# Kernel optimization log

Measured on AMD Instinct MI355X. Metric: run time of the kernel, lower is better.

Reference implementation:

```python
import jax, jax.numpy as jnp
import numpy as np

S = 2048
HIDDEN = 4096
NH, NKV, HD = 32, 8, 128
QPK = NH // NKV  # 4
BLOCK, LOCAL, VERT = 64, 16, 8
ROPE_BASE = 1.0e6
SCALE = 1.0 / HD  # mup scaling: head_dim / mup_attn_multiplier(=1.0)


def setup_inputs() -> dict:
    key = jax.random.key(0)
    ks = jax.random.split(key, 5)
    qkv_out = NKV * (QPK + 2) * HD  # 6144, head-major layout
    return {
        "positions": jnp.arange(S, dtype=jnp.int32),
        "hidden_states": jax.random.normal(ks[0], (S, HIDDEN), jnp.float32),
        "w_qkv": jax.random.normal(ks[1], (qkv_out, HIDDEN), jnp.float32) * 0.02,
        "b_qkv": jax.random.normal(ks[2], (qkv_out,), jnp.float32) * 0.02,
        "w_dense": jax.random.normal(ks[3], (HIDDEN, HIDDEN), jnp.float32) * 0.02,
        "b_dense": jax.random.normal(ks[4], (HIDDEN,), jnp.float32) * 0.02,
    }


def _rope(x, cos, sin):
    # NeoX-style (non-interleaved) rotary over full head_dim.
    # x: [S, n_heads, HD]; cos/sin: [S, HD//2]
    d2 = x.shape[-1] // 2
    x1, x2 = x[..., :d2], x[..., d2:]
    c, s = cos[:, None, :], sin[:, None, :]
    return jnp.concatenate([x1 * c - x2 * s, x2 * c + x1 * s], axis=-1)


def _blocksparse_mask(positions):
    # vllm phi3small pattern: block (qb,kb) active iff causal AND
    # (qb-kb < local_blocks OR (kb + head + 1) % vert_stride == 0), hetero heads.
    qb = positions // BLOCK                       # [S]
    heads = jnp.arange(NH, dtype=positions.dtype)
    diff = qb[:, None] - qb[None, :]              # [S,S]
    local = diff < LOCAL                          # [S,S]
    vert = ((qb[None, None, :] + heads[:, None, None] + 1) % VERT) == 0  # [NH,1,S]
    causal = positions[:, None] >= positions[None, :]                     # [S,S]
    return (local[None] | vert) & causal[None]    # [NH,S,S]


def reference(positions, hidden_states, w_qkv, b_qkv, w_dense, b_dense):
    seq = hidden_states.shape[0]
    qkv = hidden_states @ w_qkv.T + b_qkv                   # [S, 6144]
    qkv = qkv.reshape(seq, NKV, QPK + 2, HD)                # head-major split
    q = qkv[:, :, :QPK].reshape(seq, NH, HD)
    k = qkv[:, :, QPK]                                      # [S, NKV, HD]
    v = qkv[:, :, QPK + 1]

    pos = positions.astype(jnp.float32)  # rope_position_scale = 1.0
    inv_freq = 1.0 / (ROPE_BASE ** (jnp.arange(0, HD, 2, dtype=jnp.float32) / HD))
    freqs = pos[:, None] * inv_freq                          # [S, HD/2]
    cos, sin = jnp.cos(freqs), jnp.sin(freqs)
    q = _rope(q, cos, sin)
    k = _rope(k, cos, sin)

    # GQA: each kv head serves QPK query heads
    kx = jnp.repeat(k, QPK, axis=1)                          # [S, NH, HD]
    vx = jnp.repeat(v, QPK, axis=1)

    scores = jnp.einsum('qhd,khd->hqk', q, kx) * SCALE       # [NH,S,S]
    mask = _blocksparse_mask(positions)
    scores = jnp.where(mask, scores, -jnp.inf)  # diag always in local block -> no empty rows
    p = jax.nn.softmax(scores, axis=-1)
    out = jnp.einsum('hqk,khd->qhd', p, vx).reshape(seq, NH * HD)
    return out @ w_dense.T + b_dense
```

## Files before the change

### kernel.cpp

```cpp
#include <hip/hip_runtime.h>

#define S_LEN   2048
#define HID     4096
#define NHEADS  32
#define NKVH    8
#define HDIM    128
#define NQKV    6144
#define ATT_SCALE (1.0f/128.0f)

typedef unsigned short u16;
typedef __attribute__((ext_vector_type(8))) __bf16 bf16x8;
typedef __attribute__((ext_vector_type(4))) float  f32x4;

__device__ __forceinline__ u16 f2bf(float f) {
    union { float f; unsigned u; } x; x.f = f;
    unsigned u = x.u;
    u += 0x7fffu + ((u >> 16) & 1u);
    return (u16)(u >> 16);
}
__device__ __forceinline__ float bf2f(u16 v) {
    union { unsigned u; float f; } x; x.u = ((unsigned)v) << 16; return x.f;
}

__global__ __launch_bounds__(256) void cvt_bf16_kernel(const float* __restrict__ in,
                                                       u16* __restrict__ out, int n4) {
    int stride = gridDim.x * blockDim.x;
    for (int i = blockIdx.x * blockDim.x + threadIdx.x; i < n4; i += stride) {
        float4 v = *(const float4*)(in + (size_t)i * 4);
        ushort4 o = make_ushort4(f2bf(v.x), f2bf(v.y), f2bf(v.z), f2bf(v.w));
        *(ushort4*)(out + (size_t)i * 4) = o;
    }
}

#define GFENCE() asm volatile("" ::: "memory")
#define GSBAR()  do { GFENCE(); __builtin_amdgcn_s_barrier(); GFENCE(); } while (0)

template <int BN_, int NB_, bool OUT_BF16>
__global__ __launch_bounds__(512, 2) void gemm_fc_kernel(
    const u16* __restrict__ A,
    const u16* __restrict__ B,
    const float* __restrict__ bias,
    void* __restrict__ Cout,
    int M, int N, int K)
{
    constexpr int LB = BN_ / 128;
    constexpr int VM = 2 + LB;
    __shared__ u16 lds[16384 + 2 * BN_ * 64];

    const int tid  = threadIdx.x;
    const int wid  = tid >> 6;
    const int lane = tid & 63;
    const int ln   = lane & 15;
    const int quad = lane >> 4;
    const int wr   = wid >> 2;
    const int wc   = wid & 3;
    const int tileM = blockIdx.y * 128;
    const int tileN = blockIdx.x * BN_;

    f32x4 acc[2][NB_][4];
    #pragma unroll
    for (int b = 0; b < 2; b++)
        #pragma unroll
        for (int n = 0; n < NB_; n++)
            #pragma unroll
            for (int m = 0; m < 4; m++) {
                f32x4 z = {0.f, 0.f, 0.f, 0.f};
                acc[b][n][m] = z;
            }

    const int srho = lane >> 3;
    const int scol = (((lane & 7) ^ srho) << 3);

    auto gload = [&](const u16* src, u16* dst) {
        __builtin_amdgcn_global_load_lds(
            (const __attribute__((address_space(1))) void*)src,
            (__attribute__((address_space(3))) void*)dst, 16, 0, 0);
    };
    auto stage_A = [&](int kk, int bb) {
        const int base = bb * 8192;
        #pragma unroll
        for (int s = 0; s < 2; s++) {
            const int rho0 = s * 64 + wid * 8;
            const int rho  = rho0 + srho;
            const u16* src = A + (size_t)(tileM + rho) * K + (size_t)kk * 64 + scol;
            gload(src, &lds[base + rho0 * 64]);
        }
    };
    auto stage_Bh = [&](int h, int kk, int bb) {
        const int base = 16384 + bb * (BN_ * 64) + h * ((BN_ / 2) * 64);
        #pragma unroll
        for (int s = 0; s < LB; s++) {
            const int rho0 = s * 64 + wid * 8;
            const int rho  = rho0 + srho;
            const u16* src = B + (size_t)(tileN + h * (BN_ / 2) + rho) * K
                               + (size_t)kk * 64 + scol;
            gload(src, &lds[base + rho0 * 64]);
        }
    };

#define WAIT_VM()                                                                   \
    do {                                                                            \
        if constexpr (VM == 5) asm volatile("s_waitcnt vmcnt(5)" ::: "memory");     \
        else                   asm volatile("s_waitcnt vmcnt(4)" ::: "memory");     \
    } while (0)

#define READ_A()                                                                    \
    do {                                                                            \
        _Pragma("unroll")                                                           \
        for (int m = 0; m < 4; m++) {                                               \
            const int ra = wr * 64 + m * 16 + ln;                                   \
            const int ab = buf * 8192 + ra * 64;                                    \
            const int rx = ra & 7;                                                  \
            af[m][0] = *(const bf16x8*)(&lds[ab + ((quad ^ rx) << 3)]);             \
            af[m][1] = *(const bf16x8*)(&lds[ab + (((4 + quad) ^ rx) << 3)]);       \
        }                                                                           \
    } while (0)

#define MFMA_B(b_)                                                                  \
    do {                                                                            \
        __builtin_amdgcn_s_setprio(1);                                              \
        _Pragma("unroll")                                                           \
        for (int n = 0; n < NB_; n++) {                                             \
            const int rb = (b_) * (BN_ / 2) + wc * (NB_ * 16) + n * 16 + ln;        \
            const int bb = 16384 + buf * (BN_ * 64) + rb * 64;                      \
            const int rx = rb & 7;                                                  \
            bf16x8 b0 = *(const bf16x8*)(&lds[bb + ((quad ^ rx) << 3)]);            \
            bf16x8 b1 = *(const bf16x8*)(&lds[bb + (((4 + quad) ^ rx) << 3)]);      \
            _Pragma("unroll")                                                       \
            for (int m = 0; m < 4; m++) {                                           \
                acc[b_][n][m] = __builtin_amdgcn_mfma_f32_16x16x32_bf16(            \
                    af[m][0], b0, acc[b_][n][m], 0, 0, 0);                          \
                acc[b_][n][m] = __builtin_amdgcn_mfma_f32_16x16x32_bf16(            \
                    af[m][1], b1, acc[b_][n][m], 0, 0, 0);                          \
            }                                                                       \
        }                                                                           \
        __builtin_amdgcn_s_setprio(0);                                              \
    } while (0)

    const int nIter = K / 64;

    stage_A(0, 0); stage_Bh(0, 0, 0); stage_Bh(1, 0, 0);

    bf16x8 af[4][2];

    for (int t = 0; t < nIter; t++) {
        const int buf = t & 1;
        const int bn  = buf ^ 1;
        const int kn  = (t + 1 == nIter) ? 0 : t + 1;

        stage_A(kn, bn);
        WAIT_VM();
        GSBAR();
        READ_A();
        MFMA_B(0);

        stage_Bh(0, kn, bn);
        WAIT_VM();
        GSBAR();
        MFMA_B(1);
        stage_Bh(1, kn, bn);

        asm volatile("s_waitcnt lgkmcnt(0)" ::: "memory");
        GSBAR();
    }

    asm volatile("s_waitcnt vmcnt(0)" ::: "memory");

#undef WAIT_VM
#undef READ_A
#undef MFMA_B

    #pragma unroll
    for (int b = 0; b < 2; b++)
        #pragma unroll
        for (int n = 0; n < NB_; n++) {
            const int col = tileN + b * (BN_ / 2) + wc * (NB_ * 16) + n * 16 + ln;
            const float bv = bias[col];
            #pragma unroll
            for (int m = 0; m < 4; m++) {
                #pragma unroll
                for (int r = 0; r < 4; r++) {
                    const int row = tileM + wr * 64 + m * 16 + quad * 4 + r;
                    float v = acc[b][n][m][r] + bv;
                    if (OUT_BF16)
                        ((u16*)Cout)[(size_t)row * N + col] = f2bf(v);
                    else
                        ((float*)Cout)[(size_t)row * N + col] = v;
                }
            }
        }
}

__global__ __launch_bounds__(128) void rope_split_kernel(
    const u16* __restrict__ qkv, const int* __restrict__ positions,
    u16* __restrict__ qb_o, u16* __restrict__ kb_o)
{
    const int d   = threadIdx.x;
    const int pos = blockIdx.x;
    const int hy  = blockIdx.y;
    const float p = (float)positions[pos];

    const u16* src;
    u16* dst;
    if (hy < NHEADS) {
        int kv = hy >> 2, qi = hy & 3;
        src = qkv + (size_t)pos * NQKV + (kv * 6 + qi) * HDIM;
        dst = qb_o + ((size_t)hy * S_LEN + pos) * HDIM;
    } else {
        int kv = hy - NHEADS;
        src = qkv + (size_t)pos * NQKV + (kv * 6 + 4) * HDIM;
        dst = kb_o + ((size_t)kv * S_LEN + pos) * HDIM;
    }
    int d2 = d & 63;
    float inv = expf(-(float)d2 * (13.815510557964274f / 64.0f));
    float fr = p * inv;
    float s, c;
    sincosf(fr, &s, &c);
    float x1 = bf2f(src[d2]);
    float x2 = bf2f(src[d2 + 64]);
    float o = (d < 64) ? (x1 * c - x2 * s) : (x2 * c + x1 * s);
    dst[d] = f2bf(o);
}

__global__ __launch_bounds__(256) void vtrans_kernel(
    const u16* __restrict__ qkv,
    u16* __restrict__ VT)
{
    __shared__ u16 T[64][HDIM + 8];
    const int s0 = blockIdx.x * 64;
    const int kv = blockIdx.y;
    const int tid = threadIdx.x;
    #pragma unroll
    for (int p = 0; p < 4; p++) {
        int pos = p * 16 + (tid >> 4);
        int d   = (tid & 15) * 8;
        *(uint4*)&T[pos][d] =
            *(const uint4*)(qkv + (size_t)(s0 + pos) * NQKV + (kv * 6 + 5) * HDIM + d);
    }
    __syncthreads();
    #pragma unroll
    for (int p = 0; p < 4; p++) {
        int d  = p * 32 + (tid >> 3);
        int sc = (tid & 7) * 8;
        u16 tmp[8];
        #pragma unroll
        for (int j = 0; j < 8; j++) tmp[j] = T[sc + j][d];
        *(uint4*)(VT + ((size_t)kv * HDIM + d) * S_LEN + s0 + sc) = *(uint4*)tmp;
    }
}

__global__ __launch_bounds__(512, 4) void attn_bs_kernel(
    const u16* __restrict__ Q,
    const u16* __restrict__ K,
    const u16* __restrict__ V,
    u16* __restrict__ O)
{
    __shared__ u16 Ks[64 * 128];
    __shared__ u16 Vt[128 * 64];
    __shared__ u16 Ps[8][16 * 64];

    const int blk = (int)gridDim.x - 1 - (int)blockIdx.x;
    const int h   = blockIdx.y;
    const int kv  = h >> 2;
    const int tid  = threadIdx.x;
    const int w    = tid >> 6;
    const int lane = tid & 63;
    const int ln   = lane & 15;
    const int quad = lane >> 4;
    const int qbw  = 2 * blk + (w >> 2);
    const int rb16 = (w & 3) * 16;

    bf16x8 aq[4];
    {
        const u16* Qg = Q + ((size_t)h * S_LEN + qbw * 64 + rb16 + ln) * HDIM + quad * 8;
        #pragma unroll
        for (int ks = 0; ks < 4; ks++)
            aq[ks] = *(const bf16x8*)(Qg + ks * 32);
    }

    f32x4 oacc[8];
    #pragma unroll
    for (int n = 0; n < 8; n++) { f32x4 z = {0.f,0.f,0.f,0.f}; oacc[n] = z; }
    float mrow[4] = {-1e30f, -1e30f, -1e30f, -1e30f};
    float lrow[4] = {0.f, 0.f, 0.f, 0.f};

    const int kbMax = 2 * blk + 1;
    for (int kb = 0; kb <= kbMax; kb++) {
        const bool vert = (((kb + h + 1) & 7) == 0);
        const bool selu = ((kbMax - kb) < 17) || vert;
        if (!selu) continue;

        __syncthreads();

        const u16* Kg  = K + ((size_t)kv * S_LEN + kb * 64) * HDIM;
        const u16* VTg = V + (size_t)kv * HDIM * S_LEN + kb * 64;

        #pragma unroll
        for (int p = 0; p < 2; p++) {
            int r0  = w * 8 + p * 4;
            int row = r0 + (lane >> 4);
            const u16* src = Kg + (size_t)row * HDIM + (((lane & 15) ^ (row & 7)) << 3);
            __builtin_amdgcn_global_load_lds(
                (const __attribute__((address_space(1))) void*)src,
                (__attribute__((address_space(3))) void*)&Ks[r0 * 128], 16, 0, 0);
        }
        #pragma unroll
        for (int p = 0; p < 2; p++) {
            int r0  = w * 16 + p * 8;
            int row = r0 + (lane >> 3);
            int c   = (lane & 7) ^ (row & 7);
            const u16* src = VTg + (size_t)row * S_LEN + c * 8;
            __builtin_amdgcn_global_load_lds(
                (const __attribute__((address_space(1))) void*)src,
                (__attribute__((address_space(3))) void*)&Vt[r0 * 64], 16, 0, 0);
        }
        __syncthreads();

        const bool mine = (kb <= qbw) && (((qbw - kb) < 16) || vert);
        if (mine) {
            f32x4 sacc[4];
            #pragma unroll
            for (int jj = 0; jj < 4; jj++) { f32x4 z = {0.f,0.f,0.f,0.f}; sacc[jj] = z; }
            __builtin_amdgcn_s_setprio(1);
            #pragma unroll
            for (int ks = 0; ks < 4; ks++) {
                #pragma unroll
                for (int jj = 0; jj < 4; jj++) {
                    bf16x8 bk = *(const bf16x8*)(
                        &Ks[(jj * 16 + ln) * 128 + (((ks * 4 + quad) ^ (ln & 7)) << 3)]);
                    sacc[jj] = __builtin_amdgcn_mfma_f32_16x16x32_bf16(aq[ks], bk, sacc[jj], 0, 0, 0);
                }
            }
            __builtin_amdgcn_s_setprio(0);

            const bool diag = (kb == qbw);
            float pv[4][4], mxr[4];
            bool grow = false;
            #pragma unroll
            for (int r = 0; r < 4; r++) {
                const int qrow = rb16 + quad * 4 + r;
                float mx = -1e30f;
                #pragma unroll
                for (int jj = 0; jj < 4; jj++) {
                    float s = sacc[jj][r] * ATT_SCALE;
                    if (diag && (jj * 16 + ln) > qrow) s = -1e30f;
                    pv[r][jj] = s;
                    mx = fmaxf(mx, s);
                }
                #pragma unroll
                for (int off = 1; off < 16; off <<= 1)
                    mx = fmaxf(mx, __shfl_xor(mx, off, 64));
                mxr[r] = mx;
                grow |= (mx > mrow[r] + 8.0f);
            }
            if (__any(grow)) {
                #pragma unroll
                for (int r = 0; r < 4; r++) {
                    float mnew  = fmaxf(mrow[r], mxr[r]);
                    float alpha = __expf(mrow[r] - mnew);
                    lrow[r] *= alpha;
                    mrow[r]  = mnew;
                    #pragma unroll
                    for (int n = 0; n < 8; n++) oacc[n][r] *= alpha;
                }
            }
            #pragma unroll
            for (int r = 0; r < 4; r++) {
                float sum = 0.f;
                #pragma unroll
                for (int jj = 0; jj < 4; jj++) {
                    float pe = __expf(pv[r][jj] - mrow[r]);
                    pv[r][jj] = pe;
                    sum += pe;
                }
                #pragma unroll
                for (int off = 1; off < 16; off <<= 1)
                    sum += __shfl_xor(sum, off, 64);
                lrow[r] += sum;
                const int prow = quad * 4 + r;
                #pragma unroll
                for (int jj = 0; jj < 4; jj++)
                    Ps[w][prow * 64 + (((jj * 2 + (ln >> 3)) ^ (prow & 7)) << 3) + (ln & 7)]
                        = f2bf(pv[r][jj]);
            }

            __builtin_amdgcn_s_setprio(1);
            #pragma unroll
            for (int kk = 0; kk < 2; kk++) {
                bf16x8 ap = *(const bf16x8*)(
                    &Ps[w][ln * 64 + (((kk * 4 + quad) ^ (ln & 7)) << 3)]);
                #pragma unroll
                for (int n = 0; n < 8; n++) {
                    bf16x8 bv = *(const bf16x8*)(
                        &Vt[(n * 16 + ln) * 64 + (((kk * 4 + quad) ^ (ln & 7)) << 3)]);
                    oacc[n] = __builtin_amdgcn_mfma_f32_16x16x32_bf16(ap, bv, oacc[n], 0, 0, 0);
                }
            }
            __builtin_amdgcn_s_setprio(0);
        }
    }

    #pragma unroll
    for (int n = 0; n < 8; n++) {
        #pragma unroll
        for (int r = 0; r < 4; r++) {
            int pos = qbw * 64 + rb16 + quad * 4 + r;
            float o = oacc[n][r] / lrow[r];
            O[(size_t)pos * (NHEADS * HDIM) + h * HDIM + n * 16 + ln] = f2bf(o);
        }
    }
}

extern "C" void kernel_launch(void* const* d_in, const int* in_sizes, int n_in,
                              void* d_out, int out_size, void* d_ws, size_t ws_size,
                              hipStream_t stream) {
    const int*   positions = (const int*)d_in[0];
    const float* hidden    = (const float*)d_in[1];
    const float* w_qkv     = (const float*)d_in[2];
    const float* b_qkv     = (const float*)d_in[3];
    const float* w_dense   = (const float*)d_in[4];
    const float* b_dense   = (const float*)d_in[5];
    float* out = (float*)d_out;

    char* ws = (char*)d_ws;
    u16* ws_h    = (u16*)(ws);
    u16* ws_wqkv = (u16*)(ws + 16777216);
    u16* ws_wd   = (u16*)(ws + 67108864);
    u16* ws_qkv  = (u16*)(ws + 100663296);
    u16* ws_q    = (u16*)(ws + 125829120);
    u16* ws_k    = (u16*)(ws + 142606336);
    u16* ws_v    = (u16*)(ws + 146800640);
    u16* ws_attn = (u16*)(ws + 150994944);

    cvt_bf16_kernel<<<1024, 256, 0, stream>>>(hidden,  ws_h,    (S_LEN * HID) / 4);
    cvt_bf16_kernel<<<2048, 256, 0, stream>>>(w_qkv,   ws_wqkv, (NQKV * HID) / 4);
    cvt_bf16_kernel<<<2048, 256, 0, stream>>>(w_dense, ws_wd,   (HID * HID) / 4);

    gemm_fc_kernel<384, 3, true><<<dim3(NQKV / 384, S_LEN / 128), 512, 0, stream>>>(
        ws_h, ws_wqkv, b_qkv, ws_qkv, S_LEN, NQKV, HID);

    rope_split_kernel<<<dim3(S_LEN, NHEADS + NKVH), 128, 0, stream>>>(
        ws_qkv, positions, ws_q, ws_k);

    vtrans_kernel<<<dim3(S_LEN / 64, NKVH), 256, 0, stream>>>(ws_qkv, ws_v);

    attn_bs_kernel<<<dim3(S_LEN / 128, NHEADS), 512, 0, stream>>>(ws_q, ws_k, ws_v, ws_attn);

    gemm_fc_kernel<256, 2, false><<<dim3(HID / 256, S_LEN / 128), 512, 0, stream>>>(
        ws_attn, ws_wd, b_dense, out, S_LEN, HID, HID);
}
```

Baseline: 492.4 us.

## Double-buffer K/V tiles in block-sparse attention to overlap loads with MFMA

```diff
diff --git a/kernel.cpp b/kernel.cpp
--- a/kernel.cpp
+++ b/kernel.cpp
@@ -255,8 +255,8 @@
     const u16* __restrict__ V,
     u16* __restrict__ O)
 {
-    __shared__ u16 Ks[64 * 128];
-    __shared__ u16 Vt[128 * 64];
+    __shared__ u16 Ks[2][64 * 128];
+    __shared__ u16 Vt[2][128 * 64];
     __shared__ u16 Ps[8][16 * 64];
 
     const int blk = (int)gridDim.x - 1 - (int)blockIdx.x;
@@ -285,16 +285,10 @@
     float lrow[4] = {0.f, 0.f, 0.f, 0.f};
 
     const int kbMax = 2 * blk + 1;
-    for (int kb = 0; kb <= kbMax; kb++) {
-        const bool vert = (((kb + h + 1) & 7) == 0);
-        const bool selu = ((kbMax - kb) < 17) || vert;
-        if (!selu) continue;
-
-        __syncthreads();
-
+
+    auto stageKV = [&](int kb, int bb) {
         const u16* Kg  = K + ((size_t)kv * S_LEN + kb * 64) * HDIM;
         const u16* VTg = V + (size_t)kv * HDIM * S_LEN + kb * 64;
-
         #pragma unroll
         for (int p = 0; p < 2; p++) {
             int r0  = w * 8 + p * 4;
@@ -302,7 +296,7 @@
             const u16* src = Kg + (size_t)row * HDIM + (((lane & 15) ^ (row & 7)) << 3);
             __builtin_amdgcn_global_load_lds(
                 (const __attribute__((address_space(1))) void*)src,
-                (__attribute__((address_space(3))) void*)&Ks[r0 * 128], 16, 0, 0);
+                (__attribute__((address_space(3))) void*)&Ks[bb][r0 * 128], 16, 0, 0);
         }
         #pragma unroll
         for (int p = 0; p < 2; p++) {
@@ -312,10 +306,30 @@
             const u16* src = VTg + (size_t)row * S_LEN + c * 8;
             __builtin_amdgcn_global_load_lds(
                 (const __attribute__((address_space(1))) void*)src,
-                (__attribute__((address_space(3))) void*)&Vt[r0 * 64], 16, 0, 0);
-        }
-        __syncthreads();
-
+                (__attribute__((address_space(3))) void*)&Vt[bb][r0 * 64], 16, 0, 0);
+        }
+    };
+
+    auto selu_f = [&](int x) {
+        return ((kbMax - x) < 17) || (((x + h + 1) & 7) == 0);
+    };
+
+    int kb = 0;
+    while (!selu_f(kb)) kb++;
+    const int kb0 = kb;
+    stageKV(kb0, 0);
+    int cur = 0;
+
+    while (kb <= kbMax) {
+        int kn = kb + 1;
+        while (kn <= kbMax && !selu_f(kn)) kn++;
+        const bool have = (kn <= kbMax);
+
+        stageKV(have ? kn : kb0, cur ^ 1);
+        asm volatile("s_waitcnt vmcnt(4)" ::: "memory");
+        GSBAR();
+
+        const bool vert = (((kb + h + 1) & 7) == 0);
         const bool mine = (kb <= qbw) && (((qbw - kb) < 16) || vert);
         if (mine) {
             f32x4 sacc[4];
@@ -327,7 +341,7 @@
                 #pragma unroll
                 for (int jj = 0; jj < 4; jj++) {
                     bf16x8 bk = *(const bf16x8*)(
-                        &Ks[(jj * 16 + ln) * 128 + (((ks * 4 + quad) ^ (ln & 7)) << 3)]);
+                        &Ks[cur][(jj * 16 + ln) * 128 + (((ks * 4 + quad) ^ (ln & 7)) << 3)]);
                     sacc[jj] = __builtin_amdgcn_mfma_f32_16x16x32_bf16(aq[ks], bk, sacc[jj], 0, 0, 0);
                 }
             }
@@ -392,13 +406,20 @@
                 #pragma unroll
                 for (int n = 0; n < 8; n++) {
                     bf16x8 bv = *(const bf16x8*)(
-                        &Vt[(n * 16 + ln) * 64 + (((kk * 4 + quad) ^ (ln & 7)) << 3)]);
+                        &Vt[cur][(n * 16 + ln) * 64 + (((kk * 4 + quad) ^ (ln & 7)) << 3)]);
                     oacc[n] = __builtin_amdgcn_mfma_f32_16x16x32_bf16(ap, bv, oacc[n], 0, 0, 0);
                 }
             }
             __builtin_amdgcn_s_setprio(0);
         }
-    }
+
+        asm volatile("s_waitcnt lgkmcnt(0)" ::: "memory");
+        GSBAR();
+        cur ^= 1;
+        kb = have ? kn : kbMax + 1;
+    }
+
+    asm volatile("s_waitcnt vmcnt(0)" ::: "memory");
 
     #pragma unroll
     for (int n = 0; n < 8; n++) {
```

After: 496.0 us. About the same (+0.7%).
